# Kernel tuning notes

Measured on AMD Instinct MI355X. Metric: run time of the kernel, lower is better.

## Reference

```python
import jax, jax.numpy as jnp
import numpy as np


def setup_inputs() -> dict:
    key = jax.random.key(0)
    k1, k2 = jax.random.split(key)
    K, D = 512, 64
    x = jax.random.normal(k1, (64, D, 32, 32), dtype=jnp.float32)
    # torch init: uniform(-1/k, 1/k)
    weight = jax.random.uniform(k2, (D, K), dtype=jnp.float32, minval=-1.0 / K, maxval=1.0 / K)
    return {"x": x, "weight": weight}


def reference(x, weight):
    # x: [B, d, *spatial]; weight: [d, k]
    B, d = x.shape[0], x.shape[1]
    spatial = x.shape[2:]
    xf = x.reshape(B, d, -1)                      # [B, d, N]
    x2 = jnp.sum(xf * xf, axis=1)                 # [B, N]
    w2 = jnp.sum(weight * weight, axis=0)         # [k]
    dots = jnp.einsum('bdn,dk->bnk', xf, weight)  # [B, N, k]
    dist = x2[..., None] - 2.0 * dots + w2        # [B, N, k]
    argmin = jnp.argmin(dist, axis=-1)            # [B, N]
    quantized = jnp.take(weight.T, argmin, axis=0)          # [B, N, d]
    quantized = jnp.moveaxis(quantized.reshape(B, *spatial, d), -1, 1)  # [B, d, *spatial]
    return quantized, argmin.reshape(B, *spatial)
```

## Files before the change

### kernel.cpp

```cpp
#include <hip/hip_runtime.h>

#define KCODES 512
#define DDIM   64
#define NPIX   1024
#define QELEMS (64 * DDIM * NPIX)
#define PXB    32
#define NPG    (PXB / 16)
#define FLAG_GAP 4e-5f

typedef float f32x4 __attribute__((ext_vector_type(4)));
typedef short bf16x8 __attribute__((ext_vector_type(8)));
typedef unsigned int u32;
typedef u32 u32x4 __attribute__((ext_vector_type(4)));


__device__ __forceinline__ bf16x8 pack_hi(const float* f) {
  u32x4 wds;
#pragma unroll
  for (int p = 0; p < 4; ++p) {
    u32 u0 = __float_as_uint(f[2 * p]);
    u32 u1 = __float_as_uint(f[2 * p + 1]);
    wds[p] = (u0 >> 16) | (u1 & 0xffff0000u);
  }
  return __builtin_bit_cast(bf16x8, wds);
}
__device__ __forceinline__ bf16x8 pack_lo(const float* f) {
  u32x4 wds;
#pragma unroll
  for (int p = 0; p < 4; ++p) {
    float r0 = f[2 * p]     - __uint_as_float(__float_as_uint(f[2 * p])     & 0xffff0000u);
    float r1 = f[2 * p + 1] - __uint_as_float(__float_as_uint(f[2 * p + 1]) & 0xffff0000u);
    wds[p] = (__float_as_uint(r0) >> 16) | (__float_as_uint(r1) & 0xffff0000u);
  }
  return __builtin_bit_cast(bf16x8, wds);
}

__global__ void vq_prep(const float* __restrict__ w,
                        float* __restrict__ w2f_g,
                        bf16x8* __restrict__ frag) {
#pragma clang fp contract(off)
  const int blk = blockIdx.x;
  if (blk == 32) {
    int k = threadIdx.x;
    if (k < KCODES) {
      float s = 0.0f;
      for (int d = 0; d < DDIM; ++d) {
        float v = w[d * KCODES + k];
        float p = v * v;
        s = s + p;
      }
      w2f_g[k] = s;
    }
    return;
  }
  if (threadIdx.x >= 256) return;
  const int cg   = blk;
  const int t    = threadIdx.x >> 6;
  const int lane = threadIdx.x & 63;
  const int code = cg * 16 + (lane & 15);
  const int h    = t & 1;
  float f[8];
#pragma unroll
  for (int j = 0; j < 8; ++j)
    f[j] = w[(h * 32 + (lane >> 4) * 8 + j) * KCODES + code];
  frag[(cg * 4 + t) * 64 + lane] = (t < 2) ? pack_hi(f) : pack_lo(f);
}

__global__ __launch_bounds__(256) void vq_kernel(
    const float* __restrict__ x, const float* __restrict__ w,
    const float* __restrict__ w2f_g, const bf16x8* __restrict__ frag,
    float* __restrict__ qout, float* __restrict__ aout) {
#pragma clang fp contract(off)

  __shared__ float  xs[DDIM][PXB + 1];
  __shared__ float  sx2[PXB];
  __shared__ float  w2fs[KCODES];
  __shared__ float  sm1[4][PXB], sm2[4][PXB];
  __shared__ int    si1[4][PXB];
  __shared__ int    skm[PXB];
  __shared__ unsigned long long s_fmask;

  const int tid  = threadIdx.x;
  const int lane = tid & 63;
  const int lr   = lane & 15;
  const int lg   = lane >> 4;
  const int wid  = __builtin_amdgcn_readfirstlane(tid >> 6);
  const int b    = blockIdx.x >> 5;
  const int n0   = (blockIdx.x & 31) * PXB;
  const size_t pixbase = (size_t)blockIdx.x * PXB;

  {
    const float* xp = x + (size_t)b * (DDIM * NPIX) + n0;
#pragma unroll
    for (int i = 0; i < (DDIM * PXB) / 256; ++i) {
      int idx = tid + i * 256;
      int d  = idx >> 5;
      int px = idx & (PXB - 1);
      xs[d][px] = xp[(size_t)d * NPIX + px];
    }
  }
  w2fs[tid]       = w2f_g[tid];
  w2fs[tid + 256] = w2f_g[tid + 256];
  __syncthreads();

  {
    const int mypx = lane & (PXB - 1);
    float x2 = 0.0f;
#pragma unroll
    for (int d = 0; d < DDIM; ++d) {
      float xv = xs[d][mypx];
      float p = xv * xv;
      x2 = x2 + p;
    }
    if (tid < PXB) sx2[tid] = x2;
  }

  bf16x8 bxh[NPG][2], bxl[NPG][2];
#pragma unroll
  for (int pg = 0; pg < NPG; ++pg) {
#pragma unroll
    for (int h = 0; h < 2; ++h) {
      float f[8];
#pragma unroll
      for (int j = 0; j < 8; ++j)
        f[j] = xs[h * 32 + lg * 8 + j][pg * 16 + lr];
      bxh[pg][h] = pack_hi(f);
      bxl[pg][h] = pack_lo(f);
    }
  }

  float m1a[NPG], m2a[NPG];
  int   i1a[NPG];
#pragma unroll
  for (int pg = 0; pg < NPG; ++pg) { m1a[pg] = 3.4e38f; m2a[pg] = 3.4e38f; i1a[pg] = 0; }

#pragma unroll
  for (int cg = 0; cg < 8; ++cg) {
    const int codebase = wid * 128 + cg * 16;
    const bf16x8* fr = frag + (size_t)(wid * 8 + cg) * 4 * 64 + lane;
    bf16x8 awh0 = fr[0];
    bf16x8 awh1 = fr[64];
    bf16x8 awl0 = fr[128];
    bf16x8 awl1 = fr[192];

#pragma unroll
    for (int pg = 0; pg < NPG; ++pg) {
      f32x4 acc = {0.f, 0.f, 0.f, 0.f};
      acc = __builtin_amdgcn_mfma_f32_16x16x32_bf16(awh0, bxh[pg][0], acc, 0, 0, 0);
      acc = __builtin_amdgcn_mfma_f32_16x16x32_bf16(awh1, bxh[pg][1], acc, 0, 0, 0);
      acc = __builtin_amdgcn_mfma_f32_16x16x32_bf16(awl0, bxh[pg][0], acc, 0, 0, 0);
      acc = __builtin_amdgcn_mfma_f32_16x16x32_bf16(awl1, bxh[pg][1], acc, 0, 0, 0);
      acc = __builtin_amdgcn_mfma_f32_16x16x32_bf16(awh0, bxl[pg][0], acc, 0, 0, 0);
      acc = __builtin_amdgcn_mfma_f32_16x16x32_bf16(awh1, bxl[pg][1], acc, 0, 0, 0);
      acc = __builtin_amdgcn_mfma_f32_16x16x32_bf16(awl0, bxl[pg][0], acc, 0, 0, 0);
      acc = __builtin_amdgcn_mfma_f32_16x16x32_bf16(awl1, bxl[pg][1], acc, 0, 0, 0);
#pragma unroll
      for (int r = 0; r < 4; ++r) {
        int code = codebase + lg * 4 + r;
        float s = w2fs[code] - 2.0f * acc[r];
        bool lt = s < m1a[pg];
        float om1 = m1a[pg];
        m2a[pg] = lt ? om1 : fminf(s, m2a[pg]);
        m1a[pg] = lt ? s : m1a[pg];
        i1a[pg] = lt ? code : i1a[pg];
      }
    }
  }

#pragma unroll
  for (int pg = 0; pg < NPG; ++pg) {
#pragma unroll
    for (int mi = 0; mi < 2; ++mi) {
      int mask = mi ? 32 : 16;
      float pm1 = __shfl_xor(m1a[pg], mask);
      float pm2 = __shfl_xor(m2a[pg], mask);
      int   pi1 = __shfl_xor(i1a[pg], mask);
      if (pm1 < m1a[pg]) { m2a[pg] = fminf(m1a[pg], pm2); m1a[pg] = pm1; i1a[pg] = pi1; }
      else               { m2a[pg] = fminf(m2a[pg], pm1); }
    }
  }
  if (lg == 0) {
#pragma unroll
    for (int pg = 0; pg < NPG; ++pg) {
      sm1[wid][pg * 16 + lr] = m1a[pg];
      sm2[wid][pg * 16 + lr] = m2a[pg];
      si1[wid][pg * 16 + lr] = i1a[pg];
    }
  }
  __syncthreads();

  if (tid < PXB) {
    float M1 = sm1[0][tid], M2 = sm2[0][tid];
    int   I1 = si1[0][tid];
#pragma unroll
    for (int c = 1; c < 4; ++c) {
      float c1 = sm1[c][tid];
      if (c1 < M1) { M2 = fminf(M1, sm2[c][tid]); M1 = c1; I1 = si1[c][tid]; }
      else         { M2 = fminf(M2, c1); }
    }
    skm[tid] = I1;
    unsigned long long bal = __ballot(M2 - M1 < FLAG_GAP);
    if (tid == 0) s_fmask = bal;
  }
  __syncthreads();

  {
    unsigned long long fm = s_fmask;
    int idx = 0;
    while (fm) {
      const int L = __builtin_ctzll(fm);
      fm &= (fm - 1);
      if ((idx++ & 3) != wid) continue;
      const float x2L = sx2[L];
      const int k0 = lane * 8;
      float dots[8];
#pragma unroll
      for (int c = 0; c < 8; ++c) dots[c] = 0.f;
      for (int d = 0; d < DDIM; d += 4) {
        f32x4 wa[4][2];
        float xv[4];
#pragma unroll
        for (int u = 0; u < 4; ++u) {
          const float* wr = w + (size_t)(d + u) * KCODES + k0;
          wa[u][0] = *reinterpret_cast<const f32x4*>(wr);
          wa[u][1] = *reinterpret_cast<const f32x4*>(wr + 4);
          xv[u] = xs[d + u][L];
        }
#pragma unroll
        for (int u = 0; u < 4; ++u) {
#pragma unroll
          for (int c = 0; c < 4; ++c) {
            float p = xv[u] * wa[u][0][c];
            dots[c] = dots[c] + p;
          }
#pragma unroll
          for (int c = 0; c < 4; ++c) {
            float p = xv[u] * wa[u][1][c];
            dots[c + 4] = dots[c + 4] + p;
          }
        }
      }
      float bv = 3.4e38f;
      int   bi = 0;
#pragma unroll
      for (int c = 0; c < 8; ++c) {
        float t  = x2L - 2.0f * dots[c];
        float s2 = t + w2fs[k0 + c];
        if (s2 < bv) { bv = s2; bi = k0 + c; }
      }
#pragma unroll
      for (int off = 1; off < 64; off <<= 1) {
        float ov = __shfl_xor(bv, off);
        int   oi = __shfl_xor(bi, off);
        if (ov < bv || (ov == bv && oi < bi)) { bv = ov; bi = oi; }
      }
      if (lane == 0) skm[L] = bi;
    }
  }
  __syncthreads();

  if (tid < PXB) aout[pixbase + tid] = (float)skm[tid];

  {
    float* qp = qout + (size_t)b * (DDIM * NPIX) + n0;
#pragma unroll
    for (int i = 0; i < (DDIM * PXB) / 256; ++i) {
      int idx = tid + i * 256;
      int d  = idx >> 5;
      int px = idx & (PXB - 1);
      qp[(size_t)d * NPIX + px] = w[d * KCODES + skm[px]];
    }
  }
}

extern "C" void kernel_launch(void* const* d_in, const int* in_sizes, int n_in,
                              void* d_out, int out_size, void* d_ws, size_t ws_size,
                              hipStream_t stream) {
  const float* x = (const float*)d_in[0];
  const float* w = (const float*)d_in[1];
  float* qout = (float*)d_out;
  float* aout = (float*)d_out + QELEMS;

  char*   wsb   = (char*)d_ws;
  float*  w2f_g = (float*)wsb;
  bf16x8* frag  = (bf16x8*)(wsb + 4096);

  vq_prep<<<33, 512, 0, stream>>>(w, w2f_g, frag);
  vq_kernel<<<(65536 / PXB), 256, 0, stream>>>(x, w, w2f_g, frag, qout, aout);
}
```

Baseline: 50.04 us.

## Double pixels per block, transpose x tile in LDS, compute x2 lazily

Raises pixels per block from 32 to 64, so each wave's codebook fragment loads and MFMAs are reused across four pixel groups and the grid is halved. The shared x tile is stored transposed with padding so B fragments can be read with vector LDS loads. The per-pixel x-norm precompute is dropped and recomputed only for flagged pixels in the exact fallback path. In exchange, register pressure and LDS use per block go up, which may lower occupancy, and the serial fallback path does more work per flagged pixel.

New measurement: 64.42 us. 1.29x slower.

```diff
diff --git a/kernel.cpp b/kernel.cpp
--- a/kernel.cpp
+++ b/kernel.cpp
@@ -4,8 +4,9 @@
 #define DDIM   64
 #define NPIX   1024
 #define QELEMS (64 * DDIM * NPIX)
-#define PXB    32
+#define PXB    64
 #define NPG    (PXB / 16)
+#define XPAD   68
 #define FLAG_GAP 4e-5f
 
 typedef float f32x4 __attribute__((ext_vector_type(4)));
@@ -72,8 +73,7 @@
     float* __restrict__ qout, float* __restrict__ aout) {
 #pragma clang fp contract(off)
 
-  __shared__ float  xs[DDIM][PXB + 1];
-  __shared__ float  sx2[PXB];
+  __shared__ float  xs_t[PXB][XPAD];
   __shared__ float  w2fs[KCODES];
   __shared__ float  sm1[4][PXB], sm2[4][PXB];
   __shared__ int    si1[4][PXB];
@@ -85,45 +85,32 @@
   const int lr   = lane & 15;
   const int lg   = lane >> 4;
   const int wid  = __builtin_amdgcn_readfirstlane(tid >> 6);
-  const int b    = blockIdx.x >> 5;
-  const int n0   = (blockIdx.x & 31) * PXB;
+  const int b    = blockIdx.x >> 4;
+  const int n0   = (blockIdx.x & 15) * PXB;
   const size_t pixbase = (size_t)blockIdx.x * PXB;
 
   {
     const float* xp = x + (size_t)b * (DDIM * NPIX) + n0;
 #pragma unroll
-    for (int i = 0; i < (DDIM * PXB) / 256; ++i) {
-      int idx = tid + i * 256;
-      int d  = idx >> 5;
-      int px = idx & (PXB - 1);
-      xs[d][px] = xp[(size_t)d * NPIX + px];
+    for (int i = 0; i < 16; ++i) {
+      int d  = (tid >> 6) + i * 4;
+      int px = tid & 63;
+      xs_t[px][d] = xp[(size_t)d * NPIX + px];
     }
   }
   w2fs[tid]       = w2f_g[tid];
   w2fs[tid + 256] = w2f_g[tid + 256];
   __syncthreads();
 
-  {
-    const int mypx = lane & (PXB - 1);
-    float x2 = 0.0f;
-#pragma unroll
-    for (int d = 0; d < DDIM; ++d) {
-      float xv = xs[d][mypx];
-      float p = xv * xv;
-      x2 = x2 + p;
-    }
-    if (tid < PXB) sx2[tid] = x2;
-  }
-
   bf16x8 bxh[NPG][2], bxl[NPG][2];
 #pragma unroll
   for (int pg = 0; pg < NPG; ++pg) {
 #pragma unroll
     for (int h = 0; h < 2; ++h) {
-      float f[8];
-#pragma unroll
-      for (int j = 0; j < 8; ++j)
-        f[j] = xs[h * 32 + lg * 8 + j][pg * 16 + lr];
+      const float* rowp = &xs_t[pg * 16 + lr][h * 32 + lg * 8];
+      f32x4 va = *reinterpret_cast<const f32x4*>(rowp);
+      f32x4 vb = *reinterpret_cast<const f32x4*>(rowp + 4);
+      float f[8] = {va[0], va[1], va[2], va[3], vb[0], vb[1], vb[2], vb[3]};
       bxh[pg][h] = pack_hi(f);
       bxl[pg][h] = pack_lo(f);
     }
@@ -211,7 +198,12 @@
       const int L = __builtin_ctzll(fm);
       fm &= (fm - 1);
       if ((idx++ & 3) != wid) continue;
-      const float x2L = sx2[L];
+      float x2L = 0.0f;
+      for (int d = 0; d < DDIM; ++d) {
+        float xv = xs_t[L][d];
+        float p = xv * xv;
+        x2L = x2L + p;
+      }
       const int k0 = lane * 8;
       float dots[8];
 #pragma unroll
@@ -224,7 +216,7 @@
           const float* wr = w + (size_t)(d + u) * KCODES + k0;
           wa[u][0] = *reinterpret_cast<const f32x4*>(wr);
           wa[u][1] = *reinterpret_cast<const f32x4*>(wr + 4);
-          xv[u] = xs[d + u][L];
+          xv[u] = xs_t[L][d + u];
         }
 #pragma unroll
         for (int u = 0; u < 4; ++u) {
@@ -266,7 +258,7 @@
 #pragma unroll
     for (int i = 0; i < (DDIM * PXB) / 256; ++i) {
       int idx = tid + i * 256;
-      int d  = idx >> 5;
+      int d  = idx >> 6;
       int px = idx & (PXB - 1);
       qp[(size_t)d * NPIX + px] = w[d * KCODES + skm[px]];
     }
```
